# Kernel tuning notes

Hardware: AMD Instinct MI355X
Metric: run time of the kernel (lower is better)

Reference implementation:

```python
import jax, jax.numpy as jnp
import numpy as np

N = 100000
E = 1600000
NEG_SLOPE = 0.2


def _gat_layer(x, src, dst, W, a_src, a_dst, b, heads, out_ch):
    n = x.shape[0]
    h = (x @ W).reshape(n, heads, out_ch)                      # [N,H,C]
    alpha_src = (h * a_src).sum(-1)                            # [N,H]
    alpha_dst = (h * a_dst).sum(-1)                            # [N,H]
    e = jax.nn.leaky_relu(alpha_src[src] + alpha_dst[dst], NEG_SLOPE)  # [E,H]
    # segment softmax over incoming edges of each destination node
    m = jax.ops.segment_max(e, dst, num_segments=n)            # [N,H]
    ex = jnp.exp(e - m[dst])
    denom = jax.ops.segment_sum(ex, dst, num_segments=n)       # [N,H]
    alpha = ex / (denom[dst] + 1e-16)                          # [E,H]
    msg = h[src] * alpha[:, :, None]                           # [E,H,C]
    out = jax.ops.segment_sum(msg, dst, num_segments=n)        # [N,H,C]
    return out.reshape(n, heads * out_ch) + b


def setup_inputs() -> dict:
    key = jax.random.key(0)
    ks = jax.random.split(key, 10)
    glorot = lambda k, shape: jax.random.normal(k, shape, jnp.float32) * np.sqrt(2.0 / (shape[0] + shape[-1]))
    x = jax.random.normal(ks[0], (N, 5), jnp.float32)
    edge_index = jax.random.randint(ks[1], (2, E), 0, N, jnp.int64)
    return {
        "x": x,
        "edge_index": edge_index,
        "W1": glorot(ks[2], (5, 64)),
        "a_src1": glorot(ks[3], (8, 8)),
        "a_dst1": glorot(ks[4], (8, 8)),
        "b1": jnp.zeros((64,), jnp.float32),
        "W2": glorot(ks[5], (64, 2)),
        "a_src2": glorot(ks[6], (1, 2)),
        "a_dst2": glorot(ks[7], (1, 2)),
        "b2": jnp.zeros((2,), jnp.float32),
    }


def reference(x, edge_index, W1, a_src1, a_dst1, b1, W2, a_src2, a_dst2, b2):
    n = x.shape[0]
    loop = jnp.arange(n, dtype=edge_index.dtype)
    src = jnp.concatenate([edge_index[0], loop])   # PyG GATConv adds self-loops
    dst = jnp.concatenate([edge_index[1], loop])
    # dropout layers are no-ops in eval mode
    h = jax.nn.elu(_gat_layer(x, src, dst, W1, a_src1, a_dst1, b1, heads=8, out_ch=8))
    out = _gat_layer(h, src, dst, W2, a_src2, a_dst2, b2, heads=1, out_ch=2)
    return jax.nn.log_softmax(out, axis=1)
```

## Files before the change

kernel.cpp:

```cpp
#include <hip/hip_runtime.h>
#include <hip/hip_fp16.h>
#include <math.h>
#include <stdint.h>

#define N_NODES 100000
#define N_EDGES 1600000
#define N_TOT   (N_EDGES + N_NODES)
#define NEG_SLOPE 0.2f

#define CB     128
#define CBBITS 7
#define NCB    ((N_NODES + CB - 1) / CB)
#define TP     2048
#define NPB    ((N_EDGES + TP - 1) / TP)
#define WINB   2560

typedef int nt_int4 __attribute__((ext_vector_type(4)));

__global__ void k_node1(const float* __restrict__ x, const float* __restrict__ W1,
                        const float* __restrict__ a_src1, const float* __restrict__ a_dst1,
                        __half* __restrict__ h1h, __half* __restrict__ as1h,
                        float* __restrict__ ad1) {
    int tid  = blockIdx.x * blockDim.x + threadIdx.x;
    int n    = tid >> 3;
    int head = tid & 7;
    if (n >= N_NODES) return;

    float xv[5];
#pragma unroll
    for (int k = 0; k < 5; ++k) xv[k] = x[n * 5 + k];

    float hv[8];
    float as = 0.f, ad = 0.f;
#pragma unroll
    for (int j = 0; j < 8; ++j) {
        int c = head * 8 + j;
        float acc = 0.f;
#pragma unroll
        for (int k = 0; k < 5; ++k) acc += xv[k] * W1[k * 64 + c];
        hv[j] = acc;
        as += acc * a_src1[c];
        ad += acc * a_dst1[c];
    }
    __half2* hp = (__half2*)&h1h[(size_t)n * 64 + head * 8];
#pragma unroll
    for (int j = 0; j < 4; ++j)
        hp[j] = __halves2half2(__float2half(hv[2 * j]), __float2half(hv[2 * j + 1]));
    as1h[n * 8 + head] = __float2half(as);
    ad1[n * 8 + head] = ad;
}

__global__ void __launch_bounds__(512) k_part(
        const int* __restrict__ src, const int* __restrict__ dst,
        unsigned short* __restrict__ ofsT, unsigned* __restrict__ pairs) {
    __shared__ int lcnt[1024];
    __shared__ int sm[512];
    __shared__ unsigned stage[TP];
    int blk = blockIdx.x;
    int t = threadIdx.x;
    int base = blk * TP + t * 4;
    bool act = base < N_EDGES;
    int nE = min(TP, N_EDGES - blk * TP);

    lcnt[t] = 0; lcnt[t + 512] = 0;
    __syncthreads();

    nt_int4 s4, d4;
    if (act) {
        s4 = __builtin_nontemporal_load((const nt_int4*)(src + base));
        d4 = __builtin_nontemporal_load((const nt_int4*)(dst + base));
#pragma unroll
        for (int j = 0; j < 4; ++j) atomicAdd(&lcnt[d4[j] >> CBBITS], 1);
    }
    __syncthreads();

    int b0 = lcnt[t * 2], b1 = lcnt[t * 2 + 1];
    int local = b0 + b1;
    sm[t] = local;
    __syncthreads();
    for (int off = 1; off < 512; off <<= 1) {
        int u = (t >= off) ? sm[t - off] : 0;
        __syncthreads();
        sm[t] += u;
        __syncthreads();
    }
    int run = sm[t] - local;
    lcnt[t * 2] = run; lcnt[t * 2 + 1] = run + b0;
    if (t * 2     <= NCB) ofsT[(size_t)(t * 2) * NPB + blk]     = (unsigned short)run;
    if (t * 2 + 1 <= NCB) ofsT[(size_t)(t * 2 + 1) * NPB + blk] = (unsigned short)(run + b0);
    __syncthreads();

    if (act) {
#pragma unroll
        for (int j = 0; j < 4; ++j) {
            int d = d4[j], s = s4[j];
            int bin = d >> CBBITS;
            int idx = atomicAdd(&lcnt[bin], 1);
            stage[idx] = ((unsigned)(d & (CB - 1)) << 17) | (unsigned)s;
        }
    }
    __syncthreads();
    for (int i = t; i < nE; i += 512)
        pairs[(size_t)blk * TP + i] = stage[i];
}

__global__ void __launch_bounds__(512) k_csr(
        const unsigned short* __restrict__ ofsT, const unsigned* __restrict__ pairs,
        int* __restrict__ rbeg, int* __restrict__ rend, int* __restrict__ ssrc) {
    __shared__ unsigned stIn[WINB];
    __shared__ int stOut[WINB];
    __shared__ int lcnt[CB], lofs[CB], lcur[CB];
    __shared__ int wsum[2];
    __shared__ int acur;
    int B = blockIdx.x, t = threadIdx.x;
    int nvalid = min(CB, N_NODES - B * CB);
    int obase = B * WINB;

    if (t < CB) {
        lcnt[t] = (t < nvalid) ? 1 : 0;
        lcur[t] = 1;
    }
    if (t == 0) acur = 0;
    __syncthreads();

    for (int blk = t; blk < NPB; blk += 512) {
        int o0 = ofsT[(size_t)B * NPB + blk];
        int o1 = ofsT[(size_t)(B + 1) * NPB + blk];
        int n = o1 - o0;
        if (n > 0) {
            int p = atomicAdd(&acur, n);
            const unsigned* pp = pairs + (size_t)blk * TP + o0;
            for (int i = 0; i < n; ++i) {
                unsigned r = pp[i];
                stIn[p + i] = r;
                atomicAdd(&lcnt[r >> 17], 1);
            }
        }
    }
    __syncthreads();
    int m = acur;

    int v = (t < CB) ? lcnt[t] : 0;
    int ln = t & 63, wv = t >> 6;
    int sc = v;
#pragma unroll
    for (int off = 1; off < 64; off <<= 1) {
        int u = __shfl_up(sc, off, 64);
        if (ln >= off) sc += u;
    }
    if (ln == 63 && wv < 2) wsum[wv] = sc;
    __syncthreads();
    int wbase = (wv == 1) ? wsum[0] : 0;
    int ex = wbase + sc - v;
    if (t < CB) {
        lofs[t] = ex;
        int gi = B * CB + t;
        if (gi < N_NODES) {
            rbeg[gi] = obase + ex;
            rend[gi] = obase + ex + v;
            stOut[ex] = gi;
        }
    }
    __syncthreads();

    for (int k = t; k < m; k += 512) {
        unsigned p = stIn[k];
        int dl = p >> 17;
        int idx = atomicAdd(&lcur[dl], 1);
        stOut[lofs[dl] + idx] = (int)(p & 0x1FFFF);
    }
    __syncthreads();

    int tot = m + nvalid;
    for (int i = t; i < tot; i += 512) ssrc[obase + i] = stOut[i];
}

__global__ void __launch_bounds__(256) k_gather1(
        const int* __restrict__ rbeg, const int* __restrict__ rend,
        const int* __restrict__ ssrc, const float2* __restrict__ h1q,
        const __half* __restrict__ as1h, const float* __restrict__ ad1,
        const float* __restrict__ b1, const float* __restrict__ W2,
        const float* __restrict__ a_src2, const float* __restrict__ a_dst2,
        float4* __restrict__ rec) {
    int gtid = blockIdx.x * blockDim.x + threadIdx.x;
    int d    = gtid >> 6;
    int lane = threadIdx.x & 63;
    if (d >= N_NODES) return;
    int eq   = lane >> 4;
    int l    = lane & 15;
    int head = l >> 1;

    int beg = rbeg[d], end = rend[d];
    float adv = ad1[d * 8 + head];
    float a0 = 0.f, a1 = 0.f, a2 = 0.f, a3 = 0.f, den = 0.f;

    int k = beg;
    for (; k + 16 <= end; k += 16) {
        int sA = ssrc[k + eq];
        int sB = ssrc[k + 4 + eq];
        int sC = ssrc[k + 8 + eq];
        int sD = ssrc[k + 12 + eq];
        float eA = __half2float(as1h[sA * 8 + head]);
        float eB = __half2float(as1h[sB * 8 + head]);
        float eC = __half2float(as1h[sC * 8 + head]);
        float eD = __half2float(as1h[sD * 8 + head]);
        float2 rA = h1q[(size_t)sA * 16 + l];
        float2 rB = h1q[(size_t)sB * 16 + l];
        float2 rC = h1q[(size_t)sC * 16 + l];
        float2 rD = h1q[(size_t)sD * 16 + l];
        float tA = eA + adv; tA = fmaxf(tA, NEG_SLOPE * tA);
        float tB = eB + adv; tB = fmaxf(tB, NEG_SLOPE * tB);
        float tC = eC + adv; tC = fmaxf(tC, NEG_SLOPE * tC);
        float tD = eD + adv; tD = fmaxf(tD, NEG_SLOPE * tD);
        float wA = __expf(tA), wB = __expf(tB), wC = __expf(tC), wD = __expf(tD);
        float2 fA0 = __half22float2(*(__half2*)&rA.x);
        float2 fA1 = __half22float2(*(__half2*)&rA.y);
        float2 fB0 = __half22float2(*(__half2*)&rB.x);
        float2 fB1 = __half22float2(*(__half2*)&rB.y);
        float2 fC0 = __half22float2(*(__half2*)&rC.x);
        float2 fC1 = __half22float2(*(__half2*)&rC.y);
        float2 fD0 = __half22float2(*(__half2*)&rD.x);
        float2 fD1 = __half22float2(*(__half2*)&rD.y);
        a0 += wA * fA0.x + wB * fB0.x + wC * fC0.x + wD * fD0.x;
        a1 += wA * fA0.y + wB * fB0.y + wC * fC0.y + wD * fD0.y;
        a2 += wA * fA1.x + wB * fB1.x + wC * fC1.x + wD * fD1.x;
        a3 += wA * fA1.y + wB * fB1.y + wC * fC1.y + wD * fD1.y;
        den += wA + wB + wC + wD;
    }
    for (; k < end; k += 4) {
        int ki = k + eq;
        int s = ssrc[(ki < end) ? ki : beg];
        float e = __half2float(as1h[s * 8 + head]);
        float2 r = h1q[(size_t)s * 16 + l];
        float t = e + adv; t = fmaxf(t, NEG_SLOPE * t);
        float w = (ki < end) ? __expf(t) : 0.f;
        float2 f0 = __half22float2(*(__half2*)&r.x);
        float2 f1 = __half22float2(*(__half2*)&r.y);
        a0 += w * f0.x; a1 += w * f0.y;
        a2 += w * f1.x; a3 += w * f1.y;
        den += w;
    }
    a0 += __shfl_xor(a0, 16, 64);  a0 += __shfl_xor(a0, 32, 64);
    a1 += __shfl_xor(a1, 16, 64);  a1 += __shfl_xor(a1, 32, 64);
    a2 += __shfl_xor(a2, 16, 64);  a2 += __shfl_xor(a2, 32, 64);
    a3 += __shfl_xor(a3, 16, 64);  a3 += __shfl_xor(a3, 32, 64);
    den += __shfl_xor(den, 16, 64); den += __shfl_xor(den, 32, 64);

    float inv = 1.f / den;
    float4 bv = ((const float4*)b1)[l];
    float v0 = a0 * inv + bv.x;
    float v1 = a1 * inv + bv.y;
    float v2 = a2 * inv + bv.z;
    float v3 = a3 * inv + bv.w;
    v0 = (v0 > 0.f) ? v0 : (__expf(v0) - 1.f);
    v1 = (v1 > 0.f) ? v1 : (__expf(v1) - 1.f);
    v2 = (v2 > 0.f) ? v2 : (__expf(v2) - 1.f);
    v3 = (v3 > 0.f) ? v3 : (__expf(v3) - 1.f);

    float4 w2a = ((const float4*)W2)[2 * l];
    float4 w2b = ((const float4*)W2)[2 * l + 1];
    float h20 = v0 * w2a.x + v1 * w2a.z + v2 * w2b.x + v3 * w2b.z;
    float h21 = v0 * w2a.y + v1 * w2a.w + v2 * w2b.y + v3 * w2b.w;
#pragma unroll
    for (int off = 8; off; off >>= 1) {
        h20 += __shfl_xor(h20, off, 16);
        h21 += __shfl_xor(h21, off, 16);
    }
    if (lane == 0) {
        float as2v = h20 * a_src2[0] + h21 * a_src2[1];
        float ad2v = h20 * a_dst2[0] + h21 * a_dst2[1];
        rec[d] = make_float4(h20, h21, as2v, ad2v);
    }
}

__global__ void k_gather2(const int* __restrict__ rbeg, const int* __restrict__ rend,
                          const int* __restrict__ ssrc, const float4* __restrict__ rec,
                          const float* __restrict__ b2, float* __restrict__ out) {
    int gtid = blockIdx.x * blockDim.x + threadIdx.x;
    int d    = gtid >> 4;
    int lane = gtid & 15;
    if (d >= N_NODES) return;

    int beg = rbeg[d], end = rend[d];
    float adv = rec[d].w;
    float n0 = 0.f, n1 = 0.f, den = 0.f;
    int k = beg + lane;
    for (; k + 16 < end; k += 32) {
        int s0 = ssrc[k], s1 = ssrc[k + 16];
        float4 r0 = rec[s0];
        float4 r1 = rec[s1];
        float t0 = r0.z + adv; t0 = fmaxf(t0, NEG_SLOPE * t0);
        float t1 = r1.z + adv; t1 = fmaxf(t1, NEG_SLOPE * t1);
        float w0 = __expf(t0), w1 = __expf(t1);
        n0 += w0 * r0.x + w1 * r1.x;
        n1 += w0 * r0.y + w1 * r1.y;
        den += w0 + w1;
    }
    if (k < end) {
        int s = ssrc[k];
        float4 r = rec[s];
        float t = r.z + adv; t = fmaxf(t, NEG_SLOPE * t);
        float w = __expf(t);
        n0 += w * r.x; n1 += w * r.y; den += w;
    }
#pragma unroll
    for (int off = 8; off; off >>= 1) {
        n0  += __shfl_xor(n0,  off, 16);
        n1  += __shfl_xor(n1,  off, 16);
        den += __shfl_xor(den, off, 16);
    }
    if (lane == 0) {
        float o0 = n0 / den + b2[0];
        float o1 = n1 / den + b2[1];
        float m  = fmaxf(o0, o1);
        float lse = m + __logf(__expf(o0 - m) + __expf(o1 - m));
        out[d * 2 + 0] = o0 - lse;
        out[d * 2 + 1] = o1 - lse;
    }
}

extern "C" void kernel_launch(void* const* d_in, const int* in_sizes, int n_in,
                              void* d_out, int out_size, void* d_ws, size_t ws_size,
                              hipStream_t stream) {
    const float* x      = (const float*)d_in[0];
    const int*   ei     = (const int*)d_in[1];
    const float* W1     = (const float*)d_in[2];
    const float* a_src1 = (const float*)d_in[3];
    const float* a_dst1 = (const float*)d_in[4];
    const float* b1     = (const float*)d_in[5];
    const float* W2     = (const float*)d_in[6];
    const float* a_src2 = (const float*)d_in[7];
    const float* a_dst2 = (const float*)d_in[8];
    const float* b2     = (const float*)d_in[9];
    float* out = (float*)d_out;

    const int* src = ei;
    const int* dst = ei + N_EDGES;

    unsigned short* ofsT = (unsigned short*)d_ws;
    int* rbeg   = (int*)(ofsT + (size_t)(NCB + 1) * NPB);
    int* rend   = rbeg + N_NODES;
    unsigned* pairs = (unsigned*)(rend + N_NODES);
    int* ssrc   = (int*)(pairs + N_EDGES);
    uintptr_t pp = ((uintptr_t)(ssrc + (size_t)NCB * WINB) + 255) & ~(uintptr_t)255;
    float4*   rec  = (float4*)pp;
    float*    ad1  = (float*)(rec + N_NODES);
    __half*   h1h  = (__half*)(ad1 + (size_t)N_NODES * 8);
    __half*   as1h = h1h + (size_t)N_NODES * 64;

    k_node1<<<(N_NODES * 8 + 255) / 256, 256, 0, stream>>>(x, W1, a_src1, a_dst1,
                                                           h1h, as1h, ad1);
    k_part<<<NPB, 512, 0, stream>>>(src, dst, ofsT, pairs);
    k_csr<<<NCB, 512, 0, stream>>>(ofsT, pairs, rbeg, rend, ssrc);
    k_gather1<<<(N_NODES * 64 + 255) / 256, 256, 0, stream>>>(rbeg, rend, ssrc,
                                                              (const float2*)h1h,
                                                              as1h, ad1, b1, W2,
                                                              a_src2, a_dst2, rec);
    k_gather2<<<(N_NODES * 16 + 255) / 256, 256, 0, stream>>>(rbeg, rend, ssrc,
                                                              rec, b2, out);
}
```

Baseline: 182.8 us.

## Fuse CSR build with layer-1 gather, reading sources from shared memory

Merges the CSR construction kernel and the first-layer attention gather into one kernel. Each 512-thread block builds its 128-destination bucket in shared memory and then has its 8 waves aggregate those destinations directly, reading source indices from LDS instead of global memory. This removes one launch and the global read-back of ssrc/rbeg/rend for layer 1. In exchange, parallelism drops to about 782 blocks with 8 waves each looping over 16 nodes, which may hurt latency hiding for the random gathers compared with the previous one-wave-per-node launch.

```diff
diff --git a/kernel.cpp b/kernel.cpp
--- a/kernel.cpp
+++ b/kernel.cpp
@@ -104,9 +104,13 @@
         pairs[(size_t)blk * TP + i] = stage[i];
 }
 
-__global__ void __launch_bounds__(512) k_csr(
+__global__ void __launch_bounds__(512) k_bg1(
         const unsigned short* __restrict__ ofsT, const unsigned* __restrict__ pairs,
-        int* __restrict__ rbeg, int* __restrict__ rend, int* __restrict__ ssrc) {
+        const float2* __restrict__ h1q, const __half* __restrict__ as1h,
+        const float* __restrict__ ad1, const float* __restrict__ b1,
+        const float* __restrict__ W2, const float* __restrict__ a_src2,
+        const float* __restrict__ a_dst2, int* __restrict__ rbeg,
+        int* __restrict__ rend, int* __restrict__ ssrc, float4* __restrict__ rec) {
     __shared__ unsigned stIn[WINB];
     __shared__ int stOut[WINB];
     __shared__ int lcnt[CB], lofs[CB], lcur[CB];
@@ -173,103 +177,97 @@
 
     int tot = m + nvalid;
     for (int i = t; i < tot; i += 512) ssrc[obase + i] = stOut[i];
-}
-
-__global__ void __launch_bounds__(256) k_gather1(
-        const int* __restrict__ rbeg, const int* __restrict__ rend,
-        const int* __restrict__ ssrc, const float2* __restrict__ h1q,
-        const __half* __restrict__ as1h, const float* __restrict__ ad1,
-        const float* __restrict__ b1, const float* __restrict__ W2,
-        const float* __restrict__ a_src2, const float* __restrict__ a_dst2,
-        float4* __restrict__ rec) {
-    int gtid = blockIdx.x * blockDim.x + threadIdx.x;
-    int d    = gtid >> 6;
-    int lane = threadIdx.x & 63;
-    if (d >= N_NODES) return;
+
+    int lane = t & 63;
+    int wid  = t >> 6;
     int eq   = lane >> 4;
     int l    = lane & 15;
     int head = l >> 1;
 
-    int beg = rbeg[d], end = rend[d];
-    float adv = ad1[d * 8 + head];
-    float a0 = 0.f, a1 = 0.f, a2 = 0.f, a3 = 0.f, den = 0.f;
-
-    int k = beg;
-    for (; k + 16 <= end; k += 16) {
-        int sA = ssrc[k + eq];
-        int sB = ssrc[k + 4 + eq];
-        int sC = ssrc[k + 8 + eq];
-        int sD = ssrc[k + 12 + eq];
-        float eA = __half2float(as1h[sA * 8 + head]);
-        float eB = __half2float(as1h[sB * 8 + head]);
-        float eC = __half2float(as1h[sC * 8 + head]);
-        float eD = __half2float(as1h[sD * 8 + head]);
-        float2 rA = h1q[(size_t)sA * 16 + l];
-        float2 rB = h1q[(size_t)sB * 16 + l];
-        float2 rC = h1q[(size_t)sC * 16 + l];
-        float2 rD = h1q[(size_t)sD * 16 + l];
-        float tA = eA + adv; tA = fmaxf(tA, NEG_SLOPE * tA);
-        float tB = eB + adv; tB = fmaxf(tB, NEG_SLOPE * tB);
-        float tC = eC + adv; tC = fmaxf(tC, NEG_SLOPE * tC);
-        float tD = eD + adv; tD = fmaxf(tD, NEG_SLOPE * tD);
-        float wA = __expf(tA), wB = __expf(tB), wC = __expf(tC), wD = __expf(tD);
-        float2 fA0 = __half22float2(*(__half2*)&rA.x);
-        float2 fA1 = __half22float2(*(__half2*)&rA.y);
-        float2 fB0 = __half22float2(*(__half2*)&rB.x);
-        float2 fB1 = __half22float2(*(__half2*)&rB.y);
-        float2 fC0 = __half22float2(*(__half2*)&rC.x);
-        float2 fC1 = __half22float2(*(__half2*)&rC.y);
-        float2 fD0 = __half22float2(*(__half2*)&rD.x);
-        float2 fD1 = __half22float2(*(__half2*)&rD.y);
-        a0 += wA * fA0.x + wB * fB0.x + wC * fC0.x + wD * fD0.x;
-        a1 += wA * fA0.y + wB * fB0.y + wC * fC0.y + wD * fD0.y;
-        a2 += wA * fA1.x + wB * fB1.x + wC * fC1.x + wD * fD1.x;
-        a3 += wA * fA1.y + wB * fB1.y + wC * fC1.y + wD * fD1.y;
-        den += wA + wB + wC + wD;
-    }
-    for (; k < end; k += 4) {
-        int ki = k + eq;
-        int s = ssrc[(ki < end) ? ki : beg];
-        float e = __half2float(as1h[s * 8 + head]);
-        float2 r = h1q[(size_t)s * 16 + l];
-        float t = e + adv; t = fmaxf(t, NEG_SLOPE * t);
-        float w = (ki < end) ? __expf(t) : 0.f;
-        float2 f0 = __half22float2(*(__half2*)&r.x);
-        float2 f1 = __half22float2(*(__half2*)&r.y);
-        a0 += w * f0.x; a1 += w * f0.y;
-        a2 += w * f1.x; a3 += w * f1.y;
-        den += w;
-    }
-    a0 += __shfl_xor(a0, 16, 64);  a0 += __shfl_xor(a0, 32, 64);
-    a1 += __shfl_xor(a1, 16, 64);  a1 += __shfl_xor(a1, 32, 64);
-    a2 += __shfl_xor(a2, 16, 64);  a2 += __shfl_xor(a2, 32, 64);
-    a3 += __shfl_xor(a3, 16, 64);  a3 += __shfl_xor(a3, 32, 64);
-    den += __shfl_xor(den, 16, 64); den += __shfl_xor(den, 32, 64);
-
-    float inv = 1.f / den;
-    float4 bv = ((const float4*)b1)[l];
-    float v0 = a0 * inv + bv.x;
-    float v1 = a1 * inv + bv.y;
-    float v2 = a2 * inv + bv.z;
-    float v3 = a3 * inv + bv.w;
-    v0 = (v0 > 0.f) ? v0 : (__expf(v0) - 1.f);
-    v1 = (v1 > 0.f) ? v1 : (__expf(v1) - 1.f);
-    v2 = (v2 > 0.f) ? v2 : (__expf(v2) - 1.f);
-    v3 = (v3 > 0.f) ? v3 : (__expf(v3) - 1.f);
-
-    float4 w2a = ((const float4*)W2)[2 * l];
-    float4 w2b = ((const float4*)W2)[2 * l + 1];
-    float h20 = v0 * w2a.x + v1 * w2a.z + v2 * w2b.x + v3 * w2b.z;
-    float h21 = v0 * w2a.y + v1 * w2a.w + v2 * w2b.y + v3 * w2b.w;
-#pragma unroll
-    for (int off = 8; off; off >>= 1) {
-        h20 += __shfl_xor(h20, off, 16);
-        h21 += __shfl_xor(h21, off, 16);
-    }
-    if (lane == 0) {
-        float as2v = h20 * a_src2[0] + h21 * a_src2[1];
-        float ad2v = h20 * a_dst2[0] + h21 * a_dst2[1];
-        rec[d] = make_float4(h20, h21, as2v, ad2v);
+    for (int dl = wid; dl < nvalid; dl += 8) {
+        int beg = lofs[dl];
+        int end = beg + lcur[dl];
+        int d = B * CB + dl;
+        float adv = ad1[d * 8 + head];
+        float a0 = 0.f, a1 = 0.f, a2 = 0.f, a3 = 0.f, den = 0.f;
+
+        int k = beg;
+        for (; k + 16 <= end; k += 16) {
+            int sA = stOut[k + eq];
+            int sB = stOut[k + 4 + eq];
+            int sC = stOut[k + 8 + eq];
+            int sD = stOut[k + 12 + eq];
+            float eA = __half2float(as1h[sA * 8 + head]);
+            float eB = __half2float(as1h[sB * 8 + head]);
+            float eC = __half2float(as1h[sC * 8 + head]);
+            float eD = __half2float(as1h[sD * 8 + head]);
+            float2 rA = h1q[(size_t)sA * 16 + l];
+            float2 rB = h1q[(size_t)sB * 16 + l];
+            float2 rC = h1q[(size_t)sC * 16 + l];
+            float2 rD = h1q[(size_t)sD * 16 + l];
+            float tA = eA + adv; tA = fmaxf(tA, NEG_SLOPE * tA);
+            float tB = eB + adv; tB = fmaxf(tB, NEG_SLOPE * tB);
+            float tC = eC + adv; tC = fmaxf(tC, NEG_SLOPE * tC);
+            float tD = eD + adv; tD = fmaxf(tD, NEG_SLOPE * tD);
+            float wA = __expf(tA), wB = __expf(tB), wC = __expf(tC), wD = __expf(tD);
+            float2 fA0 = __half22float2(*(__half2*)&rA.x);
+            float2 fA1 = __half22float2(*(__half2*)&rA.y);
+            float2 fB0 = __half22float2(*(__half2*)&rB.x);
+            float2 fB1 = __half22float2(*(__half2*)&rB.y);
+            float2 fC0 = __half22float2(*(__half2*)&rC.x);
+            float2 fC1 = __half22float2(*(__half2*)&rC.y);
+            float2 fD0 = __half22float2(*(__half2*)&rD.x);
+            float2 fD1 = __half22float2(*(__half2*)&rD.y);
+            a0 += wA * fA0.x + wB * fB0.x + wC * fC0.x + wD * fD0.x;
+            a1 += wA * fA0.y + wB * fB0.y + wC * fC0.y + wD * fD0.y;
+            a2 += wA * fA1.x + wB * fB1.x + wC * fC1.x + wD * fD1.x;
+            a3 += wA * fA1.y + wB * fB1.y + wC * fC1.y + wD * fD1.y;
+            den += wA + wB + wC + wD;
+        }
+        for (; k < end; k += 4) {
+            int ki = k + eq;
+            int s = stOut[(ki < end) ? ki : beg];
+            float e = __half2float(as1h[s * 8 + head]);
+            float2 r = h1q[(size_t)s * 16 + l];
+            float tt = e + adv; tt = fmaxf(tt, NEG_SLOPE * tt);
+            float w = (ki < end) ? __expf(tt) : 0.f;
+            float2 f0 = __half22float2(*(__half2*)&r.x);
+            float2 f1 = __half22float2(*(__half2*)&r.y);
+            a0 += w * f0.x; a1 += w * f0.y;
+            a2 += w * f1.x; a3 += w * f1.y;
+            den += w;
+        }
+        a0 += __shfl_xor(a0, 16, 64);  a0 += __shfl_xor(a0, 32, 64);
+        a1 += __shfl_xor(a1, 16, 64);  a1 += __shfl_xor(a1, 32, 64);
+        a2 += __shfl_xor(a2, 16, 64);  a2 += __shfl_xor(a2, 32, 64);
+        a3 += __shfl_xor(a3, 16, 64);  a3 += __shfl_xor(a3, 32, 64);
+        den += __shfl_xor(den, 16, 64); den += __shfl_xor(den, 32, 64);
+
+        float inv = 1.f / den;
+        float4 bv = ((const float4*)b1)[l];
+        float v0 = a0 * inv + bv.x;
+        float v1 = a1 * inv + bv.y;
+        float v2 = a2 * inv + bv.z;
+        float v3 = a3 * inv + bv.w;
+        v0 = (v0 > 0.f) ? v0 : (__expf(v0) - 1.f);
+        v1 = (v1 > 0.f) ? v1 : (__expf(v1) - 1.f);
+        v2 = (v2 > 0.f) ? v2 : (__expf(v2) - 1.f);
+        v3 = (v3 > 0.f) ? v3 : (__expf(v3) - 1.f);
+
+        float4 w2a = ((const float4*)W2)[2 * l];
+        float4 w2b = ((const float4*)W2)[2 * l + 1];
+        float h20 = v0 * w2a.x + v1 * w2a.z + v2 * w2b.x + v3 * w2b.z;
+        float h21 = v0 * w2a.y + v1 * w2a.w + v2 * w2b.y + v3 * w2b.w;
+#pragma unroll
+        for (int off = 8; off; off >>= 1) {
+            h20 += __shfl_xor(h20, off, 16);
+            h21 += __shfl_xor(h21, off, 16);
+        }
+        if (lane == 0) {
+            float as2v = h20 * a_src2[0] + h21 * a_src2[1];
+            float ad2v = h20 * a_dst2[0] + h21 * a_dst2[1];
+            rec[d] = make_float4(h20, h21, as2v, ad2v);
+        }
     }
 }
 
@@ -351,11 +349,8 @@
     k_node1<<<(N_NODES * 8 + 255) / 256, 256, 0, stream>>>(x, W1, a_src1, a_dst1,
                                                            h1h, as1h, ad1);
     k_part<<<NPB, 512, 0, stream>>>(src, dst, ofsT, pairs);
-    k_csr<<<NCB, 512, 0, stream>>>(ofsT, pairs, rbeg, rend, ssrc);
-    k_gather1<<<(N_NODES * 64 + 255) / 256, 256, 0, stream>>>(rbeg, rend, ssrc,
-                                                              (const float2*)h1h,
-                                                              as1h, ad1, b1, W2,
-                                                              a_src2, a_dst2, rec);
+    k_bg1<<<NCB, 512, 0, stream>>>(ofsT, pairs, (const float2*)h1h, as1h, ad1,
+                                   b1, W2, a_src2, a_dst2, rbeg, rend, ssrc, rec);
     k_gather2<<<(N_NODES * 16 + 255) / 256, 256, 0, stream>>>(rbeg, rend, ssrc,
                                                               rec, b2, out);
 }
```

After: 181.8 us. Within noise of the previous version (-0.5%).
